# Kernel tuning notes

Hardware: AMD Instinct MI355X
Metric: run time of the kernel (lower is better)

The kernel has to match this reference:

```python
import jax, jax.numpy as jnp
import numpy as np

WIN = 11
SIGMA = 1.5
C1 = 0.01 ** 2
C2 = 0.03 ** 2

def _gaussian_window(channel):
    x = np.arange(WIN)
    g = np.exp(-((x - WIN // 2) ** 2) / (2.0 * SIGMA ** 2))
    g = g / g.sum()
    w2d = np.outer(g, g).astype(np.float32)  # [11,11]
    # depthwise kernel: [C, 1, 11, 11] in OIHW with feature_group_count=C
    return jnp.asarray(np.broadcast_to(w2d, (channel, 1, WIN, WIN)).copy())

def _dwconv(x, w, channel):
    pad = WIN // 2
    return jax.lax.conv_general_dilated(
        x, w, window_strides=(1, 1), padding=[(pad, pad), (pad, pad)],
        dimension_numbers=('NCHW', 'OIHW', 'NCHW'),
        feature_group_count=channel)

def _ssim(img1, img2, window, channel):
    mu1 = _dwconv(img1, window, channel)
    mu2 = _dwconv(img2, window, channel)
    mu1_sq = mu1 * mu1
    mu2_sq = mu2 * mu2
    mu1_mu2 = mu1 * mu2
    sigma1_sq = _dwconv(img1 * img1, window, channel) - mu1_sq
    sigma2_sq = _dwconv(img2 * img2, window, channel) - mu2_sq
    sigma12 = _dwconv(img1 * img2, window, channel) - mu1_mu2
    ssim_map = ((2 * mu1_mu2 + C1) * (2 * sigma12 + C2)) / (
        (mu1_sq + mu2_sq + C1) * (sigma1_sq + sigma2_sq + C2))
    return ssim_map.mean()

def setup_inputs() -> dict:
    key = jax.random.key(0)
    kA, kB, kF = jax.random.split(key, 3)
    shape = (16, 3, 512, 512)
    return {
        'image_A': jax.random.uniform(kA, shape, dtype=jnp.float32),
        'image_B': jax.random.uniform(kB, shape, dtype=jnp.float32),
        'image_fused': jax.random.uniform(kF, shape, dtype=jnp.float32),
    }

def reference(image_A, image_B, image_fused):
    channel = image_A.shape[1]
    window = _gaussian_window(channel).astype(image_A.dtype)
    loss = 0.5 * _ssim(image_A, image_fused, window, channel) \
         + 0.5 * _ssim(image_B, image_fused, window, channel)
    return loss
```

## Files before the change

kernel.cpp:

```cpp
#include <hip/hip_runtime.h>
#include <math.h>

#define IMG_W 512
#define IMG_H 512
#define NPLANES 48
#define RROWS 32
#define NCHUNK 16
#define NSTRIP 8
#define WPB 4
#define NGROUP (NCHUNK / WPB)
#define NBLOCKS (NPLANES * NSTRIP * NGROUP)
#define SSIM_C1 1e-4f
#define SSIM_C2 9e-4f

struct GW { float g[11]; };

__device__ __forceinline__ float fdiv_fast(float n, float d) {
  float r = __builtin_amdgcn_rcpf(d);
  r = r * fmaf(-d, r, 2.0f);
  float q = n * r;
  q = fmaf(fmaf(-d, q, n), r, q);
  return q;
}

__global__ __launch_bounds__(256, 2) void ssim_main(
    const float* __restrict__ A, const float* __restrict__ B,
    const float* __restrict__ F, double* __restrict__ partials, GW gw)
{
  __shared__ float sA[WPB][2][80], sB[WPB][2][80], sF[WPB][2][80];
  __shared__ double sred[WPB];
  const int b = blockIdx.x;
  const int plane = b / (NSTRIP * NGROUP);
  const int rem   = b % (NSTRIP * NGROUP);
  const int strip = rem / NGROUP;
  const int grp   = rem % NGROUP;
  const int wid = threadIdx.x >> 6;
  const int t   = threadIdx.x & 63;
  const int chunk = grp * WPB + wid;
  const int x0 = strip * 64;
  const int y0 = chunk * RROWS;
  const size_t pbase = (size_t)plane * (IMG_W * IMG_H);
  const float* Ap = A + pbase;
  const float* Bp = B + pbase;
  const float* Fp = F + pbase;

  float (&mA)[2][80] = sA[wid];
  float (&mB)[2][80] = sB[wid];
  float (&mF)[2][80] = sF[wid];

  const int c  = x0 - 5 + t;
  const bool cok = (c >= 0) && (c < IMG_W);
  const int c2 = c + 64;
  const bool c2ok = (t < 10) && (c2 < IMG_W);

  float ring[7][11];
  #pragma unroll
  for (int s = 0; s < 7; ++s)
    #pragma unroll
    for (int k = 0; k < 11; ++k) ring[s][k] = 0.f;

  float acc = 0.f;

  float rA, rB, rF, xA, xB, xF;
  auto load_row = [&](int ii) {
    const int yin = y0 - 5 + ii;
    const bool rok = (yin >= 0) && (yin < IMG_H);
    const size_t roff = (size_t)yin * IMG_W;
    rA = (rok && cok) ? Ap[roff + c] : 0.f;
    rB = (rok && cok) ? Bp[roff + c] : 0.f;
    rF = (rok && cok) ? Fp[roff + c] : 0.f;
    xA = (rok && c2ok) ? Ap[roff + c2] : 0.f;
    xB = (rok && c2ok) ? Bp[roff + c2] : 0.f;
    xF = (rok && c2ok) ? Fp[roff + c2] : 0.f;
  };

  load_row(0);

  for (int jj = 0; jj < 4; ++jj) {
    #pragma unroll
    for (int ph = 0; ph < 11; ++ph) {
      const int ii = jj * 11 + ph;
      if (ii <= RROWS + 9) {
        const int buf = ii & 1;
        mA[buf][t] = rA; mB[buf][t] = rB; mF[buf][t] = rF;
        if (t < 10) { mA[buf][t+64] = xA; mB[buf][t+64] = xB; mF[buf][t+64] = xF; }
        if (ii < RROWS + 9) load_row(ii + 1);
        float hA=0,hB=0,hF=0,hA2=0,hB2=0,hF2=0,hAF=0,hBF=0;
        #pragma unroll
        for (int k = 0; k < 11; ++k) {
          const float w = gw.g[k];
          const float a = mA[buf][t+k], bb = mB[buf][t+k], f = mF[buf][t+k];
          const float wa = w*a, wb = w*bb, wf = w*f;
          hA += wa; hB += wb; hF += wf;
          hA2 = fmaf(wa, a, hA2); hB2 = fmaf(wb, bb, hB2); hF2 = fmaf(wf, f, hF2);
          hAF = fmaf(wa, f, hAF); hBF = fmaf(wb, f, hBF);
        }
        ring[0][ph]=hA;  ring[1][ph]=hB;  ring[2][ph]=hF;
        ring[3][ph]=hA2+hF2;  ring[4][ph]=hB2+hF2;
        ring[5][ph]=hAF; ring[6][ph]=hBF;

        if (ii >= 10) {
          float m[7];
          #pragma unroll
          for (int s = 0; s < 7; ++s) m[s] = 0.f;
          #pragma unroll
          for (int k = 0; k < 11; ++k) {
            const int sl = (ph + 1 + k) % 11;
            const float w = gw.g[k];
            #pragma unroll
            for (int s = 0; s < 7; ++s) m[s] = fmaf(w, ring[s][sl], m[s]);
          }
          const float mAv=m[0], mBv=m[1], mFv=m[2];
          const float vS1=m[3], vS2=m[4], vAF=m[5], vBF=m[6];
          const float mA2=mAv*mAv, mB2=mBv*mBv, mF2=mFv*mFv,
                      mAF=mAv*mFv, mBF=mBv*mFv;
          const float sAF = vAF - mAF, sBF = vBF - mBF;
          const float ts1 = vS1 - mA2 - mF2;
          const float ts2 = vS2 - mB2 - mF2;
          const float n1 = fmaf(2.f, mAF, SSIM_C1) * fmaf(2.f, sAF, SSIM_C2);
          const float d1 = (mA2 + mF2 + SSIM_C1) * (ts1 + SSIM_C2);
          const float n2 = fmaf(2.f, mBF, SSIM_C1) * fmaf(2.f, sBF, SSIM_C2);
          const float d2 = (mB2 + mF2 + SSIM_C1) * (ts2 + SSIM_C2);
          acc += fdiv_fast(n1, d1) + fdiv_fast(n2, d2);
        }
      }
    }
  }

  float wsum = acc;
  #pragma unroll
  for (int off = 32; off > 0; off >>= 1)
    wsum += __shfl_down(wsum, off, 64);
  if (t == 0) sred[wid] = (double)wsum;
  __syncthreads();
  if (threadIdx.x == 0)
    partials[b] = sred[0] + sred[1] + sred[2] + sred[3];
}

__global__ __launch_bounds__(256) void ssim_final(
    const double* __restrict__ partials, float* __restrict__ out)
{
  __shared__ double sd[256];
  const int t = threadIdx.x;
  double s = 0.0;
  for (int i = t; i < NBLOCKS; i += 256) s += partials[i];
  sd[t] = s;
  __syncthreads();
  for (int off = 128; off > 0; off >>= 1) {
    if (t < off) sd[t] += sd[t + off];
    __syncthreads();
  }
  if (t == 0)
    out[0] = (float)(0.5 * sd[0] / (double)(16.0 * 3.0 * 512.0 * 512.0));
}

extern "C" void kernel_launch(void* const* d_in, const int* in_sizes, int n_in,
                              void* d_out, int out_size, void* d_ws, size_t ws_size,
                              hipStream_t stream) {
  const float* A = (const float*)d_in[0];
  const float* B = (const float*)d_in[1];
  const float* F = (const float*)d_in[2];
  double* partials = (double*)d_ws;

  GW gw;
  double g[11], s = 0.0;
  for (int i = 0; i < 11; ++i) { g[i] = exp(-((double)((i-5)*(i-5))) / 4.5); s += g[i]; }
  for (int i = 0; i < 11; ++i) gw.g[i] = (float)(g[i] / s);

  hipLaunchKernelGGL(ssim_main, dim3(NBLOCKS), dim3(WPB * 64), 0, stream,
                     A, B, F, partials, gw);
  hipLaunchKernelGGL(ssim_final, dim3(1), dim3(256), 0, stream,
                     partials, (float*)d_out);
}
```

Baseline: 239.2 us.

## Process two rows per step with packed float2 math and a paired ring buffer

Restructures the row loop so each step loads, stages and horizontally filters two image rows at once, using 2-wide float vectors meant to map to packed FP32 instructions (v_pk_fma_f32) on CDNA. The vertical ring buffer now holds row pairs (6 slots × 2), and the vertical filter produces two output rows per step. This halves loop iterations and shared-memory store/sync steps and aims to double ALU throughput via packed ops. In exchange it raises register pressure from twice as many in-flight loads and 2-wide accumulators, which could hurt occupancy.

```diff
diff --git a/kernel.cpp b/kernel.cpp
--- a/kernel.cpp
+++ b/kernel.cpp
@@ -13,7 +13,14 @@
 #define SSIM_C1 1e-4f
 #define SSIM_C2 9e-4f
 
+typedef float f32x2 __attribute__((ext_vector_type(2)));
+
 struct GW { float g[11]; };
+
+__device__ __forceinline__ f32x2 splat2(float v) { return (f32x2){v, v}; }
+__device__ __forceinline__ f32x2 fma2(f32x2 a, f32x2 b, f32x2 c) {
+  return __builtin_elementwise_fma(a, b, c);
+}
 
 __device__ __forceinline__ float fdiv_fast(float n, float d) {
   float r = __builtin_amdgcn_rcpf(d);
@@ -27,7 +34,7 @@
     const float* __restrict__ A, const float* __restrict__ B,
     const float* __restrict__ F, double* __restrict__ partials, GW gw)
 {
-  __shared__ float sA[WPB][2][80], sB[WPB][2][80], sF[WPB][2][80];
+  __shared__ float sA[WPB][2][2][80], sB[WPB][2][2][80], sF[WPB][2][2][80];
   __shared__ double sred[WPB];
   const int b = blockIdx.x;
   const int plane = b / (NSTRIP * NGROUP);
@@ -44,84 +51,112 @@
   const float* Bp = B + pbase;
   const float* Fp = F + pbase;
 
-  float (&mA)[2][80] = sA[wid];
-  float (&mB)[2][80] = sB[wid];
-  float (&mF)[2][80] = sF[wid];
+  float (&mA)[2][2][80] = sA[wid];
+  float (&mB)[2][2][80] = sB[wid];
+  float (&mF)[2][2][80] = sF[wid];
 
   const int c  = x0 - 5 + t;
   const bool cok = (c >= 0) && (c < IMG_W);
   const int c2 = c + 64;
   const bool c2ok = (t < 10) && (c2 < IMG_W);
 
-  float ring[7][11];
+  f32x2 ring[7][6];
   #pragma unroll
   for (int s = 0; s < 7; ++s)
     #pragma unroll
-    for (int k = 0; k < 11; ++k) ring[s][k] = 0.f;
+    for (int k = 0; k < 6; ++k) ring[s][k] = splat2(0.f);
 
   float acc = 0.f;
 
-  float rA, rB, rF, xA, xB, xF;
-  auto load_row = [&](int ii) {
-    const int yin = y0 - 5 + ii;
-    const bool rok = (yin >= 0) && (yin < IMG_H);
-    const size_t roff = (size_t)yin * IMG_W;
-    rA = (rok && cok) ? Ap[roff + c] : 0.f;
-    rB = (rok && cok) ? Bp[roff + c] : 0.f;
-    rF = (rok && cok) ? Fp[roff + c] : 0.f;
-    xA = (rok && c2ok) ? Ap[roff + c2] : 0.f;
-    xB = (rok && c2ok) ? Bp[roff + c2] : 0.f;
-    xF = (rok && c2ok) ? Fp[roff + c2] : 0.f;
+  float rA0,rB0,rF0,xA0,xB0,xF0, rA1,rB1,rF1,xA1,xB1,xF1;
+  auto load_pair = [&](int ii) {
+    const int yin0 = y0 - 5 + 2*ii;
+    const int yin1 = yin0 + 1;
+    const bool r0 = (yin0 >= 0) && (yin0 < IMG_H);
+    const bool r1 = (yin1 >= 0) && (yin1 < IMG_H);
+    const size_t o0 = (size_t)yin0 * IMG_W;
+    const size_t o1 = (size_t)yin1 * IMG_W;
+    rA0 = (r0 && cok) ? Ap[o0 + c] : 0.f;
+    rB0 = (r0 && cok) ? Bp[o0 + c] : 0.f;
+    rF0 = (r0 && cok) ? Fp[o0 + c] : 0.f;
+    rA1 = (r1 && cok) ? Ap[o1 + c] : 0.f;
+    rB1 = (r1 && cok) ? Bp[o1 + c] : 0.f;
+    rF1 = (r1 && cok) ? Fp[o1 + c] : 0.f;
+    xA0 = (r0 && c2ok) ? Ap[o0 + c2] : 0.f;
+    xB0 = (r0 && c2ok) ? Bp[o0 + c2] : 0.f;
+    xF0 = (r0 && c2ok) ? Fp[o0 + c2] : 0.f;
+    xA1 = (r1 && c2ok) ? Ap[o1 + c2] : 0.f;
+    xB1 = (r1 && c2ok) ? Bp[o1 + c2] : 0.f;
+    xF1 = (r1 && c2ok) ? Fp[o1 + c2] : 0.f;
   };
 
-  load_row(0);
+  load_pair(0);
 
   for (int jj = 0; jj < 4; ++jj) {
     #pragma unroll
-    for (int ph = 0; ph < 11; ++ph) {
-      const int ii = jj * 11 + ph;
-      if (ii <= RROWS + 9) {
+    for (int ph = 0; ph < 6; ++ph) {
+      const int ii = jj * 6 + ph;
+      if (ii < 21) {
         const int buf = ii & 1;
-        mA[buf][t] = rA; mB[buf][t] = rB; mF[buf][t] = rF;
-        if (t < 10) { mA[buf][t+64] = xA; mB[buf][t+64] = xB; mF[buf][t+64] = xF; }
-        if (ii < RROWS + 9) load_row(ii + 1);
-        float hA=0,hB=0,hF=0,hA2=0,hB2=0,hF2=0,hAF=0,hBF=0;
+        mA[buf][0][t] = rA0; mA[buf][1][t] = rA1;
+        mB[buf][0][t] = rB0; mB[buf][1][t] = rB1;
+        mF[buf][0][t] = rF0; mF[buf][1][t] = rF1;
+        if (t < 10) {
+          mA[buf][0][t+64] = xA0; mA[buf][1][t+64] = xA1;
+          mB[buf][0][t+64] = xB0; mB[buf][1][t+64] = xB1;
+          mF[buf][0][t+64] = xF0; mF[buf][1][t+64] = xF1;
+        }
+        if (ii < 20) load_pair(ii + 1);
+        f32x2 hA=splat2(0.f), hB=splat2(0.f), hF=splat2(0.f),
+              hA2=splat2(0.f), hB2=splat2(0.f), hF2=splat2(0.f),
+              hAF=splat2(0.f), hBF=splat2(0.f);
         #pragma unroll
         for (int k = 0; k < 11; ++k) {
           const float w = gw.g[k];
-          const float a = mA[buf][t+k], bb = mB[buf][t+k], f = mF[buf][t+k];
-          const float wa = w*a, wb = w*bb, wf = w*f;
+          const f32x2 a  = {mA[buf][0][t+k], mA[buf][1][t+k]};
+          const f32x2 bb = {mB[buf][0][t+k], mB[buf][1][t+k]};
+          const f32x2 f  = {mF[buf][0][t+k], mF[buf][1][t+k]};
+          const f32x2 wv = splat2(w);
+          const f32x2 wa = wv*a, wb = wv*bb, wf = wv*f;
           hA += wa; hB += wb; hF += wf;
-          hA2 = fmaf(wa, a, hA2); hB2 = fmaf(wb, bb, hB2); hF2 = fmaf(wf, f, hF2);
-          hAF = fmaf(wa, f, hAF); hBF = fmaf(wb, f, hBF);
+          hA2 = fma2(wa, a, hA2); hB2 = fma2(wb, bb, hB2); hF2 = fma2(wf, f, hF2);
+          hAF = fma2(wa, f, hAF); hBF = fma2(wb, f, hBF);
         }
         ring[0][ph]=hA;  ring[1][ph]=hB;  ring[2][ph]=hF;
         ring[3][ph]=hA2+hF2;  ring[4][ph]=hB2+hF2;
         ring[5][ph]=hAF; ring[6][ph]=hBF;
 
-        if (ii >= 10) {
-          float m[7];
+        if (ii >= 5) {
+          f32x2 M[7];
           #pragma unroll
-          for (int s = 0; s < 7; ++s) m[s] = 0.f;
+          for (int s = 0; s < 7; ++s) M[s] = splat2(0.f);
           #pragma unroll
           for (int k = 0; k < 11; ++k) {
-            const int sl = (ph + 1 + k) % 11;
             const float w = gw.g[k];
+            const int plo = (ph + 1 + (k >> 1)) % 6;
+            const int phi = (ph + 1 + ((k + 1) >> 1)) % 6;
             #pragma unroll
-            for (int s = 0; s < 7; ++s) m[s] = fmaf(w, ring[s][sl], m[s]);
+            for (int s = 0; s < 7; ++s) {
+              const float elo = (k & 1)       ? ring[s][plo].y : ring[s][plo].x;
+              const float ehi = ((k + 1) & 1) ? ring[s][phi].y : ring[s][phi].x;
+              M[s].x = fmaf(w, elo, M[s].x);
+              M[s].y = fmaf(w, ehi, M[s].y);
+            }
           }
-          const float mAv=m[0], mBv=m[1], mFv=m[2];
-          const float vS1=m[3], vS2=m[4], vAF=m[5], vBF=m[6];
-          const float mA2=mAv*mAv, mB2=mBv*mBv, mF2=mFv*mFv,
+          const f32x2 mAv=M[0], mBv=M[1], mFv=M[2];
+          const f32x2 vS1=M[3], vS2=M[4], vAF=M[5], vBF=M[6];
+          const f32x2 mA2=mAv*mAv, mB2=mBv*mBv, mF2=mFv*mFv,
                       mAF=mAv*mFv, mBF=mBv*mFv;
-          const float sAF = vAF - mAF, sBF = vBF - mBF;
-          const float ts1 = vS1 - mA2 - mF2;
-          const float ts2 = vS2 - mB2 - mF2;
-          const float n1 = fmaf(2.f, mAF, SSIM_C1) * fmaf(2.f, sAF, SSIM_C2);
-          const float d1 = (mA2 + mF2 + SSIM_C1) * (ts1 + SSIM_C2);
-          const float n2 = fmaf(2.f, mBF, SSIM_C1) * fmaf(2.f, sBF, SSIM_C2);
-          const float d2 = (mB2 + mF2 + SSIM_C1) * (ts2 + SSIM_C2);
-          acc += fdiv_fast(n1, d1) + fdiv_fast(n2, d2);
+          const f32x2 sAFv = vAF - mAF, sBFv = vBF - mBF;
+          const f32x2 ts1 = vS1 - mA2 - mF2;
+          const f32x2 ts2 = vS2 - mB2 - mF2;
+          const f32x2 two = splat2(2.f), c1 = splat2(SSIM_C1), c2v = splat2(SSIM_C2);
+          const f32x2 n1 = fma2(two, mAF, c1) * fma2(two, sAFv, c2v);
+          const f32x2 d1 = (mA2 + mF2 + c1) * (ts1 + c2v);
+          const f32x2 n2 = fma2(two, mBF, c1) * fma2(two, sBFv, c2v);
+          const f32x2 d2 = (mB2 + mF2 + c1) * (ts2 + c2v);
+          acc += fdiv_fast(n1.x, d1.x) + fdiv_fast(n2.x, d2.x);
+          acc += fdiv_fast(n1.y, d1.y) + fdiv_fast(n2.y, d2.y);
         }
       }
     }
```

Measured after the change: 215.2 us. 10.0% less time.
